# Performance work log

Measured on AMD Instinct MI355X. Metric: run time of the kernel, lower is better.

The kernel has to match this reference:

```python
import jax, jax.numpy as jnp
import numpy as np

HEADS = 8
DIM_HEAD = 32
SCALE = DIM_HEAD ** -0.5


def setup_inputs() -> dict:
    key = jax.random.key(0)
    k1, k2, k3 = jax.random.split(key, 3)
    B, L, H, W, C = 2, 5, 100, 176, 256
    inner = HEADS * DIM_HEAD  # 256
    x = jax.random.normal(k1, (B, L, H, W, C), dtype=jnp.float32)
    mask = jnp.ones((B, H, W, 1, L), dtype=jnp.float32)
    W_qkv = jax.random.normal(k2, (C, 3 * inner), dtype=jnp.float32) * (C ** -0.5)
    W_out = jax.random.normal(k3, (inner, C), dtype=jnp.float32) * (inner ** -0.5)
    b_out = jnp.zeros((C,), dtype=jnp.float32)
    return {"x": x, "mask": mask, "W_qkv": W_qkv, "W_out": W_out, "b_out": b_out}


def _cav_attention(x, mask, W_qkv, W_out, b_out):
    B, L, H, W, C = x.shape
    # (B, L, H, W, C) -> (B, H, W, L, C)
    xp = jnp.transpose(x, (0, 2, 3, 1, 4))
    qkv = xp @ W_qkv  # (B,H,W,L,3*inner)
    q, k, v = jnp.split(qkv, 3, axis=-1)

    def to_heads(t):  # (B,H,W,L,m*c) -> (B,m,H,W,L,c)
        t = t.reshape(B, H, W, L, HEADS, DIM_HEAD)
        return jnp.transpose(t, (0, 4, 1, 2, 3, 5))

    q, k, v = to_heads(q), to_heads(k), to_heads(v)
    att = jnp.einsum('bmhwic,bmhwjc->bmhwij', q, k) * SCALE
    # mask: (B,H,W,1,L) -> broadcast over heads as (B,1,H,W,1,L)
    att = jnp.where(mask[:, None] == 0, -jnp.inf, att)
    att = jax.nn.softmax(att, axis=-1)
    out = jnp.einsum('bmhwij,bmhwjc->bmhwic', att, v)
    # (B,m,H,W,L,c) -> (B,H,W,L,m*c)
    out = jnp.transpose(out, (0, 2, 3, 4, 1, 5)).reshape(B, H, W, L, HEADS * DIM_HEAD)
    out = out @ W_out + b_out  # dropout is identity in eval mode
    # (B,H,W,L,C) -> (B,L,H,W,C)
    return jnp.transpose(out, (0, 3, 1, 2, 4))


def reference(x, mask, W_qkv, W_out, b_out):
    return _cav_attention(x, mask, W_qkv, W_out, b_out)
```

## Files before the change

### kernel.cpp

```cpp
#include <hip/hip_runtime.h>
#include <hip/hip_bf16.h>

#define LQ 5
#define HWQ 17600
#define NT 35200
#define TPB 8
#define ROWS 40
#define NBLK 4400
#define SCALE_QK 0.17677669529663687f

#define AO_OFF 0
#define WAVE_OFF 20480
#define WAVE_STRIDE 10368
#define VT_OFF 5760
#define GOFS_OFF 61952
#define MASK_OFF 62144
#define SMEM_BYTES 62336

typedef __attribute__((ext_vector_type(8))) short bf16x8;
typedef __attribute__((ext_vector_type(4))) float f32x4;

__device__ __forceinline__ unsigned short f2bf(float f) {
  __hip_bfloat16 b = __float2bfloat16(f);
  return *(unsigned short*)&b;
}
__device__ __forceinline__ unsigned pack2(float a, float b) {
  return ((unsigned)f2bf(b) << 16) | (unsigned)f2bf(a);
}
__device__ __forceinline__ int swzA(int row, int b) { return (row * 512 + b) ^ ((row & 7) << 4); }
__device__ __forceinline__ int swzR(int row, int off) { return row * 144 + (off ^ ((row & 3) << 4)); }

__global__ void prep_weights(const float* __restrict__ Wqkv,
                             const float* __restrict__ Wout,
                             unsigned short* __restrict__ WqkvT,
                             unsigned short* __restrict__ WoutT) {
  int idx = blockIdx.x * 256 + threadIdx.x;
  if (idx < 256 * 768) {
    int k = idx / 768, n = idx - k * 768;
    WqkvT[n * 256 + k] = f2bf(Wqkv[idx]);
  }
  if (idx < 256 * 256) {
    int k = idx >> 8, n = idx & 255;
    WoutT[n * 256 + k] = f2bf(Wout[idx]);
  }
}

__device__ __forceinline__ void do_head(int head, const char* AO, char* qkp, char* vt,
                                        const unsigned short* __restrict__ WqkvT,
                                        const f32x4* mrg ,
                                        int lr, int lg, int lane,
                                        f32x4* oacc ) {
  const int hb = head * 32;
  const unsigned short* bp[6];
  bp[0] = WqkvT + (hb + lr) * 256 + lg * 8;
  bp[1] = WqkvT + (hb + 16 + lr) * 256 + lg * 8;
  bp[2] = WqkvT + (256 + hb + lr) * 256 + lg * 8;
  bp[3] = WqkvT + (256 + hb + 16 + lr) * 256 + lg * 8;
  bp[4] = WqkvT + (512 + hb + lr) * 256 + lg * 8;
  bp[5] = WqkvT + (512 + hb + 16 + lr) * 256 + lg * 8;

  f32x4 aqk[4][3], av[2][3];
  #pragma unroll
  for (int j = 0; j < 4; ++j)
    #pragma unroll
    for (int g = 0; g < 3; ++g) aqk[j][g] = (f32x4){0.f, 0.f, 0.f, 0.f};
  #pragma unroll
  for (int j = 0; j < 2; ++j)
    #pragma unroll
    for (int g = 0; g < 3; ++g) av[j][g] = (f32x4){0.f, 0.f, 0.f, 0.f};

  bf16x8 bb0[6], bb1[6];
  #pragma unroll
  for (int j = 0; j < 6; ++j) {
    bb0[j] = *(const bf16x8*)(bp[j]);
    bb1[j] = *(const bf16x8*)(bp[j] + 32);
  }

  #pragma unroll
  for (int kt = 0; kt < 8; ++kt) {
    bf16x8 xf0 = *(const bf16x8*)(AO + swzA(lr,      kt * 64 + lg * 16));
    bf16x8 xf1 = *(const bf16x8*)(AO + swzA(16 + lr, kt * 64 + lg * 16));
    bf16x8 xf2 = *(const bf16x8*)(AO + swzA(32 + lr, kt * 64 + lg * 16));
    #pragma unroll
    for (int j = 0; j < 4; ++j) {
      bf16x8 w = (kt & 1) ? bb1[j] : bb0[j];
      aqk[j][0] = __builtin_amdgcn_mfma_f32_16x16x32_bf16(w, xf0, aqk[j][0], 0, 0, 0);
      aqk[j][1] = __builtin_amdgcn_mfma_f32_16x16x32_bf16(w, xf1, aqk[j][1], 0, 0, 0);
      aqk[j][2] = __builtin_amdgcn_mfma_f32_16x16x32_bf16(w, xf2, aqk[j][2], 0, 0, 0);
    }
    #pragma unroll
    for (int j = 0; j < 2; ++j) {
      bf16x8 w = (kt & 1) ? bb1[4 + j] : bb0[4 + j];
      av[j][0] = __builtin_amdgcn_mfma_f32_16x16x32_bf16(xf0, w, av[j][0], 0, 0, 0);
      av[j][1] = __builtin_amdgcn_mfma_f32_16x16x32_bf16(xf1, w, av[j][1], 0, 0, 0);
      av[j][2] = __builtin_amdgcn_mfma_f32_16x16x32_bf16(xf2, w, av[j][2], 0, 0, 0);
    }
    if (kt < 6) {
      #pragma unroll
      for (int j = 0; j < 6; ++j) {
        bf16x8 nl = *(const bf16x8*)(bp[j] + (kt + 2) * 32);
        if (kt & 1) bb1[j] = nl; else bb0[j] = nl;
      }
    }
  }

  #pragma unroll
  for (int j = 0; j < 4; ++j)
    #pragma unroll
    for (int g = 0; g < 3; ++g) {
      int sp = g * 16 + lr;
      if (sp < ROWS) {
        uint2 w;
        w.x = pack2(aqk[j][g][0], aqk[j][g][1]);
        w.y = pack2(aqk[j][g][2], aqk[j][g][3]);
        int off = (j & 1) * 32 + lg * 8 + ((j >= 2) ? 64 : 0);
        *(uint2*)(qkp + swzR(sp, off)) = w;
      }
    }
  #pragma unroll
  for (int j = 0; j < 2; ++j)
    #pragma unroll
    for (int g = 0; g < 3; ++g) {
      if (g < 2 || lg < 2) {
        uint2 w;
        w.x = pack2(av[j][g][0], av[j][g][1]);
        w.y = pack2(av[j][g][2], av[j][g][3]);
        *(uint2*)(vt + swzR(j * 16 + lr, g * 32 + lg * 8)) = w;
      }
    }

  bf16x8 kf0 = *(const bf16x8*)(qkp + swzR(lr,      64 + lg * 16));
  bf16x8 kf1 = *(const bf16x8*)(qkp + swzR(16 + lr, 64 + lg * 16));
  bf16x8 kf2 = *(const bf16x8*)(qkp + swzR(32 + lr, 64 + lg * 16));
  f32x4 sa[3][3];
  #pragma unroll
  for (int gq = 0; gq < 3; ++gq) {
    bf16x8 qf = *(const bf16x8*)(qkp + swzR(gq * 16 + lr, lg * 16));
    sa[gq][0] = __builtin_amdgcn_mfma_f32_16x16x32_bf16(kf0, qf, (f32x4){0.f,0.f,0.f,0.f}, 0, 0, 0);
    sa[gq][1] = __builtin_amdgcn_mfma_f32_16x16x32_bf16(kf1, qf, (f32x4){0.f,0.f,0.f,0.f}, 0, 0, 0);
    sa[gq][2] = __builtin_amdgcn_mfma_f32_16x16x32_bf16(kf2, qf, (f32x4){0.f,0.f,0.f,0.f}, 0, 0, 0);
  }

  if (lane < ROWS) {
    *(uint4*)(qkp + swzR(lane, 96))  = make_uint4(0, 0, 0, 0);
    *(uint4*)(qkp + swzR(lane, 112)) = make_uint4(0, 0, 0, 0);
  }

  #pragma unroll
  for (int gq = 0; gq < 3; ++gq) {
    int q = gq * 16 + lr;
    int t5 = (q / 5) * 5;
    float v[3][4];
    #pragma unroll
    for (int gk = 0; gk < 3; ++gk)
      #pragma unroll
      for (int r = 0; r < 4; ++r) {
        int k = gk * 16 + lg * 4 + r;
        float raw = sa[gq][gk][r] * SCALE_QK + mrg[gk][r];
        v[gk][r] = ((unsigned)(k - t5) < 5u) ? raw : -1e30f;
      }
    float m = v[0][0];
    #pragma unroll
    for (int gk = 0; gk < 3; ++gk)
      #pragma unroll
      for (int r = 0; r < 4; ++r) m = fmaxf(m, v[gk][r]);
    m = fmaxf(m, __shfl_xor(m, 16));
    m = fmaxf(m, __shfl_xor(m, 32));
    float e[3][4], s = 0.f;
    #pragma unroll
    for (int gk = 0; gk < 3; ++gk)
      #pragma unroll
      for (int r = 0; r < 4; ++r) { e[gk][r] = __expf(v[gk][r] - m); s += e[gk][r]; }
    s += __shfl_xor(s, 16);
    s += __shfl_xor(s, 32);
    float inv = 1.0f / s;
    if (q < ROWS) {
      #pragma unroll
      for (int gk = 0; gk < 3; ++gk) {
        uint2 w;
        w.x = pack2(e[gk][0] * inv, e[gk][1] * inv);
        w.y = pack2(e[gk][2] * inv, e[gk][3] * inv);
        *(uint2*)(qkp + swzR(q, gk * 32 + lg * 8)) = w;
      }
    }
  }

  #pragma unroll
  for (int kt = 0; kt < 2; ++kt) {
    bf16x8 vf0 = *(const bf16x8*)(vt + swzR(lr,      kt * 64 + lg * 16));
    bf16x8 vf1 = *(const bf16x8*)(vt + swzR(16 + lr, kt * 64 + lg * 16));
    #pragma unroll
    for (int gq = 0; gq < 3; ++gq) {
      bf16x8 pf = *(const bf16x8*)(qkp + swzR(gq * 16 + lr, kt * 64 + lg * 16));
      oacc[gq * 2 + 0] = __builtin_amdgcn_mfma_f32_16x16x32_bf16(pf, vf0, oacc[gq * 2 + 0], 0, 0, 0);
      oacc[gq * 2 + 1] = __builtin_amdgcn_mfma_f32_16x16x32_bf16(pf, vf1, oacc[gq * 2 + 1], 0, 0, 0);
    }
  }
}

__global__ __launch_bounds__(256, 2)
void cav_attn_fused(const float* __restrict__ x,
                    const float* __restrict__ mask,
                    const unsigned short* __restrict__ WqkvT,
                    const unsigned short* __restrict__ WoutT,
                    const float* __restrict__ b_out,
                    float* __restrict__ out) {
  extern __shared__ char smem[];
  char*  AO    = smem + AO_OFF;
  int*   gofs  = (int*)(smem + GOFS_OFF);
  float* maskb = (float*)(smem + MASK_OFF);

  const int tid  = threadIdx.x;
  const int wave = tid >> 6;
  const int lane = tid & 63;
  const int lr   = lane & 15;
  const int lg   = lane >> 4;
  const int tile0 = blockIdx.x * TPB;

  if (lane < 48) {
    if (lane < ROWS) {
      int tt = lane / LQ;
      int l  = lane - tt * LQ;
      int gt = tile0 + tt;
      int b  = (gt >= HWQ) ? 1 : 0;
      int rem = gt - b * HWQ;
      gofs[lane]  = (((b * LQ + l) * 100) * 176 + rem) << 8;
      float mv = mask[tile0 * LQ + lane];
      maskb[lane] = (mv == 0.0f) ? -1e30f : 0.0f;
    } else {
      gofs[lane] = 0;
      maskb[lane] = 0.0f;
    }
  }

  char* qkp = smem + WAVE_OFF + wave * WAVE_STRIDE;
  char* vt  = qkp + VT_OFF;

  if (lane < 32) {
    *(uint4*)(vt + swzR(lane, 80))  = make_uint4(0, 0, 0, 0);
    *(uint4*)(vt + swzR(lane, 96))  = make_uint4(0, 0, 0, 0);
    *(uint4*)(vt + swzR(lane, 112)) = make_uint4(0, 0, 0, 0);
  }

  f32x4 mrg[3];
  #pragma unroll
  for (int gk = 0; gk < 3; ++gk)
    mrg[gk] = *(const f32x4*)(maskb + gk * 16 + lg * 4);

  #pragma unroll
  for (int i = 0; i < 10; ++i) {
    int r = i * 4 + wave;
    f32x4 v = *(const f32x4*)(x + gofs[r] + lane * 4);
    ushort4 pk;
    pk.x = f2bf(v[0]); pk.y = f2bf(v[1]); pk.z = f2bf(v[2]); pk.w = f2bf(v[3]);
    *(ushort4*)(AO + swzA(r, lane * 8)) = pk;
  }
  __syncthreads();

  f32x4 oacc0[6], oacc1[6];
  #pragma unroll
  for (int i = 0; i < 6; ++i) { oacc0[i] = (f32x4){0.f,0.f,0.f,0.f}; oacc1[i] = (f32x4){0.f,0.f,0.f,0.f}; }

  do_head(wave * 2,     AO, qkp, vt, WqkvT, mrg, lr, lg, lane, oacc0);
  do_head(wave * 2 + 1, AO, qkp, vt, WqkvT, mrg, lr, lg, lane, oacc1);

  __syncthreads();

  #pragma unroll
  for (int gq = 0; gq < 3; ++gq)
    #pragma unroll
    for (int nf = 0; nf < 2; ++nf)
      #pragma unroll
      for (int rg = 0; rg < 4; ++rg) {
        int sp = gq * 16 + lg * 4 + rg;
        if (sp < ROWS) {
          int fb0 = (wave * 64 + nf * 16 + lr) * 2;
          *(unsigned short*)(AO + swzA(sp, fb0))      = f2bf(oacc0[gq * 2 + nf][rg]);
          *(unsigned short*)(AO + swzA(sp, fb0 + 64)) = f2bf(oacc1[gq * 2 + nf][rg]);
        }
      }
  __syncthreads();

  f32x4 acc2[4][3];
  #pragma unroll
  for (int j = 0; j < 4; ++j)
    #pragma unroll
    for (int g = 0; g < 3; ++g) acc2[j][g] = (f32x4){0.f, 0.f, 0.f, 0.f};

  const unsigned short* bp2[4];
  #pragma unroll
  for (int j = 0; j < 4; ++j)
    bp2[j] = WoutT + (wave * 64 + j * 16 + lr) * 256 + lg * 8;

  bf16x8 cc0[4], cc1[4];
  #pragma unroll
  for (int j = 0; j < 4; ++j) {
    cc0[j] = *(const bf16x8*)(bp2[j]);
    cc1[j] = *(const bf16x8*)(bp2[j] + 32);
  }

  #pragma unroll
  for (int kt = 0; kt < 8; ++kt) {
    bf16x8 of0 = *(const bf16x8*)(AO + swzA(lr,      kt * 64 + lg * 16));
    bf16x8 of1 = *(const bf16x8*)(AO + swzA(16 + lr, kt * 64 + lg * 16));
    bf16x8 of2 = *(const bf16x8*)(AO + swzA(32 + lr, kt * 64 + lg * 16));
    #pragma unroll
    for (int j = 0; j < 4; ++j) {
      bf16x8 w = (kt & 1) ? cc1[j] : cc0[j];
      acc2[j][0] = __builtin_amdgcn_mfma_f32_16x16x32_bf16(w, of0, acc2[j][0], 0, 0, 0);
      acc2[j][1] = __builtin_amdgcn_mfma_f32_16x16x32_bf16(w, of1, acc2[j][1], 0, 0, 0);
      acc2[j][2] = __builtin_amdgcn_mfma_f32_16x16x32_bf16(w, of2, acc2[j][2], 0, 0, 0);
    }
    if (kt < 6) {
      #pragma unroll
      for (int j = 0; j < 4; ++j) {
        bf16x8 nl = *(const bf16x8*)(bp2[j] + (kt + 2) * 32);
        if (kt & 1) cc1[j] = nl; else cc0[j] = nl;
      }
    }
  }

  f32x4 bias[4];
  #pragma unroll
  for (int j = 0; j < 4; ++j)
    bias[j] = *(const f32x4*)(b_out + wave * 64 + j * 16 + lg * 4);

  #pragma unroll
  for (int g = 0; g < 3; ++g) {
    int sp = g * 16 + lr;
    if (sp < ROWS) {
      int go = gofs[sp];
      #pragma unroll
      for (int j = 0; j < 4; ++j) {
        f32x4 v = acc2[j][g] + bias[j];
        *(f32x4*)(out + go + wave * 64 + j * 16 + lg * 4) = v;
      }
    }
  }
}

extern "C" void kernel_launch(void* const* d_in, const int* in_sizes, int n_in,
                              void* d_out, int out_size, void* d_ws, size_t ws_size,
                              hipStream_t stream) {
  (void)in_sizes; (void)n_in; (void)out_size; (void)ws_size;
  const float* x    = (const float*)d_in[0];
  const float* mask = (const float*)d_in[1];
  const float* Wqkv = (const float*)d_in[2];
  const float* Wout = (const float*)d_in[3];
  const float* bout = (const float*)d_in[4];
  float* out = (float*)d_out;

  unsigned short* WqkvT = (unsigned short*)d_ws;
  unsigned short* WoutT = WqkvT + 768 * 256;

  prep_weights<<<768, 256, 0, stream>>>(Wqkv, Wout, WqkvT, WoutT);
  cav_attn_fused<<<NBLK, 256, SMEM_BYTES, stream>>>(x, mask, WqkvT, WoutT, bout, out);
}
```

Measured before the change: 386.7 us.

## Build V operand via cross-lane permutes instead of LDS staging, shrink LDS

Each wave no longer writes the V projection to a shared-memory transpose buffer. The MFMA B-operand fragments for the PV product are now assembled directly from registers with ds_bpermute. The per-wave scratch layout shrinks to a 128-byte-row swizzle, and LDS drops from about 62KB to 45KB per block, which could allow more resident blocks per CU. This removes the V stores and the zero-padding writes, at the cost of extra permute instructions and register pressure.

New measurement: 379.2 us. No clear change (-1.9%).

```diff
diff --git a/kernel.cpp b/kernel.cpp
--- a/kernel.cpp
+++ b/kernel.cpp
@@ -10,12 +10,11 @@
 #define SCALE_QK 0.17677669529663687f
 
 #define AO_OFF 0
-#define WAVE_OFF 20480
-#define WAVE_STRIDE 10368
-#define VT_OFF 5760
-#define GOFS_OFF 61952
-#define MASK_OFF 62144
-#define SMEM_BYTES 62336
+#define QKP_OFF 20480
+#define QKP_STRIDE 6144
+#define GOFS_OFF 45056
+#define MASK_OFF 45248
+#define SMEM_BYTES 45440
 
 typedef __attribute__((ext_vector_type(8))) short bf16x8;
 typedef __attribute__((ext_vector_type(4))) float f32x4;
@@ -28,7 +27,7 @@
   return ((unsigned)f2bf(b) << 16) | (unsigned)f2bf(a);
 }
 __device__ __forceinline__ int swzA(int row, int b) { return (row * 512 + b) ^ ((row & 7) << 4); }
-__device__ __forceinline__ int swzR(int row, int off) { return row * 144 + (off ^ ((row & 3) << 4)); }
+__device__ __forceinline__ int swz128(int row, int off) { return row * 128 + (off ^ ((row & 7) << 4)); }
 
 __global__ void prep_weights(const float* __restrict__ Wqkv,
                              const float* __restrict__ Wout,
@@ -45,7 +44,7 @@
   }
 }
 
-__device__ __forceinline__ void do_head(int head, const char* AO, char* qkp, char* vt,
+__device__ __forceinline__ void do_head(int head, const char* AO, char* qkp,
                                         const unsigned short* __restrict__ WqkvT,
                                         const f32x4* mrg ,
                                         int lr, int lg, int lane,
@@ -114,36 +113,32 @@
         w.x = pack2(aqk[j][g][0], aqk[j][g][1]);
         w.y = pack2(aqk[j][g][2], aqk[j][g][3]);
         int off = (j & 1) * 32 + lg * 8 + ((j >= 2) ? 64 : 0);
-        *(uint2*)(qkp + swzR(sp, off)) = w;
-      }
-    }
+        *(uint2*)(qkp + swz128(sp, off)) = w;
+      }
+    }
+
+  const bool lgHi = (lane >= 32);
+  unsigned pv[2][3][2];
   #pragma unroll
   for (int j = 0; j < 2; ++j)
     #pragma unroll
     for (int g = 0; g < 3; ++g) {
-      if (g < 2 || lg < 2) {
-        uint2 w;
-        w.x = pack2(av[j][g][0], av[j][g][1]);
-        w.y = pack2(av[j][g][2], av[j][g][3]);
-        *(uint2*)(vt + swzR(j * 16 + lr, g * 32 + lg * 8)) = w;
-      }
-    }
-
-  bf16x8 kf0 = *(const bf16x8*)(qkp + swzR(lr,      64 + lg * 16));
-  bf16x8 kf1 = *(const bf16x8*)(qkp + swzR(16 + lr, 64 + lg * 16));
-  bf16x8 kf2 = *(const bf16x8*)(qkp + swzR(32 + lr, 64 + lg * 16));
+      unsigned w0 = pack2(av[j][g][0], av[j][g][1]);
+      unsigned w1 = pack2(av[j][g][2], av[j][g][3]);
+      if (g == 2 && lgHi) { w0 = 0; w1 = 0; }
+      pv[j][g][0] = w0; pv[j][g][1] = w1;
+    }
+
+  bf16x8 kf0 = *(const bf16x8*)(qkp + swz128(lr,      64 + lg * 16));
+  bf16x8 kf1 = *(const bf16x8*)(qkp + swz128(16 + lr, 64 + lg * 16));
+  bf16x8 kf2 = *(const bf16x8*)(qkp + swz128(32 + lr, 64 + lg * 16));
   f32x4 sa[3][3];
   #pragma unroll
   for (int gq = 0; gq < 3; ++gq) {
-    bf16x8 qf = *(const bf16x8*)(qkp + swzR(gq * 16 + lr, lg * 16));
+    bf16x8 qf = *(const bf16x8*)(qkp + swz128(gq * 16 + lr, lg * 16));
     sa[gq][0] = __builtin_amdgcn_mfma_f32_16x16x32_bf16(kf0, qf, (f32x4){0.f,0.f,0.f,0.f}, 0, 0, 0);
     sa[gq][1] = __builtin_amdgcn_mfma_f32_16x16x32_bf16(kf1, qf, (f32x4){0.f,0.f,0.f,0.f}, 0, 0, 0);
     sa[gq][2] = __builtin_amdgcn_mfma_f32_16x16x32_bf16(kf2, qf, (f32x4){0.f,0.f,0.f,0.f}, 0, 0, 0);
-  }
-
-  if (lane < ROWS) {
-    *(uint4*)(qkp + swzR(lane, 96))  = make_uint4(0, 0, 0, 0);
-    *(uint4*)(qkp + swzR(lane, 112)) = make_uint4(0, 0, 0, 0);
   }
 
   #pragma unroll
@@ -180,20 +175,30 @@
         uint2 w;
         w.x = pack2(e[gk][0] * inv, e[gk][1] * inv);
         w.y = pack2(e[gk][2] * inv, e[gk][3] * inv);
-        *(uint2*)(qkp + swzR(q, gk * 32 + lg * 8)) = w;
-      }
-    }
-  }
-
+        *(uint2*)(qkp + swz128(q, gk * 32 + lg * 8)) = w;
+      }
+    }
+  }
+
+  const int idxA = (((lane & 16) ? 32 : 0) + lr) * 4;
+  const int idxB = idxA + 64;
   #pragma unroll
   for (int kt = 0; kt < 2; ++kt) {
-    bf16x8 vf0 = *(const bf16x8*)(vt + swzR(lr,      kt * 64 + lg * 16));
-    bf16x8 vf1 = *(const bf16x8*)(vt + swzR(16 + lr, kt * 64 + lg * 16));
+    union { unsigned u[4]; bf16x8 v; } vf[2];
+    #pragma unroll
+    for (int j = 0; j < 2; ++j)
+      #pragma unroll
+      for (int w = 0; w < 4; ++w) {
+        int idx = (w >> 1) ? idxB : idxA;
+        unsigned a = (unsigned)__builtin_amdgcn_ds_bpermute(idx, (int)pv[j][2 * kt][w & 1]);
+        unsigned b = (kt == 0) ? (unsigned)__builtin_amdgcn_ds_bpermute(idx, (int)pv[j][1][w & 1]) : 0u;
+        vf[j].u[w] = lgHi ? b : a;
+      }
     #pragma unroll
     for (int gq = 0; gq < 3; ++gq) {
-      bf16x8 pf = *(const bf16x8*)(qkp + swzR(gq * 16 + lr, kt * 64 + lg * 16));
-      oacc[gq * 2 + 0] = __builtin_amdgcn_mfma_f32_16x16x32_bf16(pf, vf0, oacc[gq * 2 + 0], 0, 0, 0);
-      oacc[gq * 2 + 1] = __builtin_amdgcn_mfma_f32_16x16x32_bf16(pf, vf1, oacc[gq * 2 + 1], 0, 0, 0);
+      bf16x8 pf = *(const bf16x8*)(qkp + swz128(gq * 16 + lr, kt * 64 + lg * 16));
+      oacc[gq * 2 + 0] = __builtin_amdgcn_mfma_f32_16x16x32_bf16(pf, vf[0].v, oacc[gq * 2 + 0], 0, 0, 0);
+      oacc[gq * 2 + 1] = __builtin_amdgcn_mfma_f32_16x16x32_bf16(pf, vf[1].v, oacc[gq * 2 + 1], 0, 0, 0);
     }
   }
 }
@@ -233,13 +238,11 @@
     }
   }
 
-  char* qkp = smem + WAVE_OFF + wave * WAVE_STRIDE;
-  char* vt  = qkp + VT_OFF;
-
-  if (lane < 32) {
-    *(uint4*)(vt + swzR(lane, 80))  = make_uint4(0, 0, 0, 0);
-    *(uint4*)(vt + swzR(lane, 96))  = make_uint4(0, 0, 0, 0);
-    *(uint4*)(vt + swzR(lane, 112)) = make_uint4(0, 0, 0, 0);
+  char* qkp = smem + QKP_OFF + wave * QKP_STRIDE;
+  {
+    int zr = 40 + (lane >> 3);
+    int zb = (lane & 7) * 16;
+    *(uint4*)(qkp + swz128(zr, zb)) = make_uint4(0, 0, 0, 0);
   }
 
   f32x4 mrg[3];
@@ -261,8 +264,8 @@
   #pragma unroll
   for (int i = 0; i < 6; ++i) { oacc0[i] = (f32x4){0.f,0.f,0.f,0.f}; oacc1[i] = (f32x4){0.f,0.f,0.f,0.f}; }
 
-  do_head(wave * 2,     AO, qkp, vt, WqkvT, mrg, lr, lg, lane, oacc0);
-  do_head(wave * 2 + 1, AO, qkp, vt, WqkvT, mrg, lr, lg, lane, oacc1);
+  do_head(wave * 2,     AO, qkp, WqkvT, mrg, lr, lg, lane, oacc0);
+  do_head(wave * 2 + 1, AO, qkp, WqkvT, mrg, lr, lg, lane, oacc1);
 
   __syncthreads();
 
```
